# Kernel tuning notes

Hardware: AMD Instinct MI355X
Metric: run time of the kernel (lower is better)

The kernel has to match this reference:

```python
import jax, jax.numpy as jnp
import numpy as np

B, H, S, Dh = 4, 16, 2048, 64
NEG = -1.0e9


def setup_inputs() -> dict:
    key = jax.random.key(0)
    kq, kk, kv = jax.random.split(key, 3)
    q = jax.random.normal(kq, (B, H, S, Dh), dtype=jnp.float32)
    k = jax.random.normal(kk, (B, H, S, Dh), dtype=jnp.float32)
    v = jax.random.normal(kv, (B, H, S, Dh), dtype=jnp.float32)
    # causal mask: 1.0 where attention is disallowed (j > i), matching mask * -1e9
    mask = jnp.triu(jnp.ones((S, S), dtype=jnp.float32), k=1)[None, None, :, :]
    return {"q": q, "k": k, "v": v, "mask": mask}


def reference(q, k, v, mask):
    # scaled dot-product attention: softmax(QK^T / sqrt(Dh) + mask * -1e9) V
    dim_k = jnp.asarray(k.shape[-1], dtype=jnp.float32)
    logits = jnp.einsum("bhsd,bhtd->bhst", q, k) / jnp.sqrt(dim_k)
    logits = logits + mask * NEG
    weights = jax.nn.softmax(logits, axis=-1)
    return jnp.einsum("bhst,bhtd->bhsd", weights, v)
```

## Files before the change

kernel.cpp:

```cpp
#include <hip/hip_runtime.h>

#define S_LEN 2048
#define DH 64

typedef float f32x4 __attribute__((ext_vector_type(4)));
typedef __bf16 bf16x8 __attribute__((ext_vector_type(8)));

#define PTS 72

__device__ __forceinline__ unsigned short f2bf(float f) {
    unsigned u = __builtin_bit_cast(unsigned, f);
    u += 0x7fffu + ((u >> 16) & 1u);
    return (unsigned short)(u >> 16);
}

__device__ __forceinline__ uint4 pack8(const float* s) {
    unsigned short h[8];
#pragma unroll
    for (int i = 0; i < 8; ++i) h[i] = f2bf(s[i]);
    return *(const uint4*)h;
}

__device__ __forceinline__ unsigned pack_tr(float a, float b) {
    return __builtin_amdgcn_perm(__builtin_bit_cast(unsigned, b),
                                 __builtin_bit_cast(unsigned, a), 0x07060302u);
}

__device__ __forceinline__ bf16x8 ld128(const unsigned short* p) {
    return __builtin_bit_cast(bf16x8, *(const uint4*)p);
}

__global__ __launch_bounds__(256) void prep_kv(const float* __restrict__ k,
                                               const float* __restrict__ v,
                                               uint4* __restrict__ kimg,
                                               uint4* __restrict__ vimg) {
    __shared__ unsigned short tr[64 * 40];
    const int bid = blockIdx.x;
    const int t = threadIdx.x;
    if (bid < 4096) {
        const int r = t >> 3, b = t & 7;
        const int srcblk = b ^ (r & 7);
        const float* src = k + ((size_t)bid * 32 + r) * 64 + srcblk * 8;
        float buf[8];
        *(float4*)&buf[0] = *(const float4*)src;
        *(float4*)&buf[4] = *(const float4*)(src + 4);
        kimg[(size_t)bid * 256 + t] = pack8(buf);
    } else {
        const int vb = bid - 4096;
        const int r = t >> 3, cb = t & 7;
        const float* src = v + ((size_t)vb * 32 + r) * 64 + cb * 8;
        float buf[8];
        *(float4*)&buf[0] = *(const float4*)src;
        *(float4*)&buf[4] = *(const float4*)(src + 4);
#pragma unroll
        for (int i = 0; i < 8; ++i)
            tr[(cb * 8 + i) * 40 + r] = f2bf(buf[i]);
        __syncthreads();
        const int d = t >> 2, kb = t & 3;
        const int skb = kb ^ ((d >> 1) & 3);
        vimg[(size_t)vb * 256 + t] = *(const uint4*)&tr[d * 40 + skb * 8];
    }
}

template <int DIAG>
__device__ __forceinline__ void body64(
    const unsigned short* __restrict__ kt, const unsigned short* __restrict__ vt,
    unsigned short* __restrict__ pw0, unsigned short* __restrict__ pw1,
    const bf16x8* qf, f32x4 acc[2][4], f32x4* accl,
    int jt, int qbase, int quad, int c)
{
    const int sw = c & 7;
    const unsigned ones_u = 0x3F803F80u;
    uint4 ou; ou.x = ones_u; ou.y = ones_u; ou.z = ones_u; ou.w = ones_u;
    const bf16x8 ones = __builtin_bit_cast(bf16x8, ou);
    const int MTN = (DIAG == 1) ? 2 : 4;

#pragma unroll
    for (int mt = 0; mt < MTN; ++mt) {
        const unsigned short* kr = kt + (mt * 16 + c) * 64;
        bf16x8 ka0 = ld128(kr + ((quad ^ sw) << 3));
        bf16x8 ka1 = ld128(kr + (((quad | 4) ^ sw) << 3));
        f32x4 s0 = (f32x4){0.f, 0.f, 0.f, 0.f};
        f32x4 s1 = (f32x4){0.f, 0.f, 0.f, 0.f};
        s0 = __builtin_amdgcn_mfma_f32_16x16x32_bf16(ka0, qf[0], s0, 0, 0, 0);
        s0 = __builtin_amdgcn_mfma_f32_16x16x32_bf16(ka1, qf[1], s0, 0, 0, 0);
        s1 = __builtin_amdgcn_mfma_f32_16x16x32_bf16(ka0, qf[2], s1, 0, 0, 0);
        s1 = __builtin_amdgcn_mfma_f32_16x16x32_bf16(ka1, qf[3], s1, 0, 0, 0);

        const bool MASKMT = (DIAG == 1) || (DIAG == 2 && mt >= 2);
#pragma unroll
        for (int s = 0; s < 2; ++s) {
            const f32x4 st = s ? s1 : s0;
            const int ig = qbase + s * 16 + c;
            float p[4];
#pragma unroll
            for (int r = 0; r < 4; ++r) {
                float e = exp2f(st[r]);
                if (MASKMT) {
                    const int jg = jt * 64 + mt * 16 + quad * 4 + r;
                    e = (jg > ig) ? 0.f : e;
                }
                p[r] = e;
            }
            unsigned a = pack_tr(p[0], p[1]);
            unsigned b = pack_tr(p[2], p[3]);
            unsigned* pb = (unsigned*)(s ? pw1 : pw0) + c * (PTS / 2) + mt * 8 + quad * 2;
            *(uint2*)pb = make_uint2(a, b);
        }
    }

    bf16x8 pf00 = ld128(pw0 + c * PTS + quad * 8);
    bf16x8 pf10 = ld128(pw1 + c * PTS + quad * 8);
    accl[0] = __builtin_amdgcn_mfma_f32_16x16x32_bf16(pf00, ones, accl[0], 0, 0, 0);
    accl[1] = __builtin_amdgcn_mfma_f32_16x16x32_bf16(pf10, ones, accl[1], 0, 0, 0);
    bf16x8 pf01, pf11;
    if (DIAG != 1) {
        pf01 = ld128(pw0 + c * PTS + 32 + quad * 8);
        pf11 = ld128(pw1 + c * PTS + 32 + quad * 8);
        accl[0] = __builtin_amdgcn_mfma_f32_16x16x32_bf16(pf01, ones, accl[0], 0, 0, 0);
        accl[1] = __builtin_amdgcn_mfma_f32_16x16x32_bf16(pf11, ones, accl[1], 0, 0, 0);
    }

    const int vsw = (c >> 1) & 3;
#pragma unroll
    for (int dc = 0; dc < 4; ++dc) {
        const unsigned short* vr = vt + (dc * 16 + c) * 32 + ((quad ^ vsw) << 3);
        bf16x8 vf0 = ld128(vr);
        acc[0][dc] = __builtin_amdgcn_mfma_f32_16x16x32_bf16(pf00, vf0, acc[0][dc], 0, 0, 0);
        acc[1][dc] = __builtin_amdgcn_mfma_f32_16x16x32_bf16(pf10, vf0, acc[1][dc], 0, 0, 0);
        if (DIAG != 1) {
            bf16x8 vf1 = ld128(vr + 2048);
            acc[0][dc] = __builtin_amdgcn_mfma_f32_16x16x32_bf16(pf01, vf1, acc[0][dc], 0, 0, 0);
            acc[1][dc] = __builtin_amdgcn_mfma_f32_16x16x32_bf16(pf11, vf1, acc[1][dc], 0, 0, 0);
        }
    }
}

__global__ __launch_bounds__(256, 4) void fa_kernel(
    const float* __restrict__ q,
    const uint4* __restrict__ kimg,
    const uint4* __restrict__ vimg,
    float* __restrict__ out)
{
    __shared__ unsigned short kt[64 * 64];
    __shared__ unsigned short vt[2 * 64 * 32];
    __shared__ unsigned short pt[4][2][16 * PTS];

    const int tid  = threadIdx.x;
    const int lane = tid & 63;
    const int wave = tid >> 6;
    const int quad = lane >> 4;
    const int c    = lane & 15;

    const int bid  = blockIdx.x;
    const int bh   = bid & 63;
    const int qblk = bid >> 6;

    const int wt      = qblk * 4 + wave;
    const int qbase   = wt * 32;
    const int my_diag = wt >> 1;
    const int jt_last = 2 * qblk + 1;

    const size_t head_off = (size_t)bh * S_LEN * DH;

    const float SCALE = 0.125f * 1.4426950408889634f;
    bf16x8 qf[4];
#pragma unroll
    for (int s = 0; s < 2; ++s) {
        const float* qrow = q + head_off + (size_t)(qbase + s * 16 + c) * DH;
        float t0[8], t1[8];
#pragma unroll
        for (int i = 0; i < 8; ++i) t0[i] = qrow[quad * 8 + i] * SCALE;
#pragma unroll
        for (int i = 0; i < 8; ++i) t1[i] = qrow[32 + quad * 8 + i] * SCALE;
        qf[s * 2 + 0] = __builtin_bit_cast(bf16x8, pack8(t0));
        qf[s * 2 + 1] = __builtin_bit_cast(bf16x8, pack8(t1));
    }

    f32x4 acc[2][4];
#pragma unroll
    for (int s = 0; s < 2; ++s)
#pragma unroll
        for (int dc = 0; dc < 4; ++dc) acc[s][dc] = (f32x4){0.f, 0.f, 0.f, 0.f};
    f32x4 accl[2];
    accl[0] = (f32x4){0.f, 0.f, 0.f, 0.f};
    accl[1] = (f32x4){0.f, 0.f, 0.f, 0.f};

    const uint4* kin = kimg + (size_t)bh * 64 * 256 + tid;
    const uint4* vin = vimg + (size_t)bh * 64 * 256 + tid;
    unsigned short* pw0 = pt[wave][0];
    unsigned short* pw1 = pt[wave][1];

    uint4 kA = kin[0], kB = kin[256];
    uint4 vA = vin[0], vB = vin[256];
    for (int jt = 0; jt <= jt_last; ++jt) {
        __syncthreads();
        ((uint4*)kt)[tid] = kA;  ((uint4*)kt)[tid + 256] = kB;
        ((uint4*)vt)[tid] = vA;  ((uint4*)vt)[tid + 256] = vB;
        if (jt < jt_last) {
            kA = kin[(jt + 1) * 512];  kB = kin[(jt + 1) * 512 + 256];
            vA = vin[(jt + 1) * 512];  vB = vin[(jt + 1) * 512 + 256];
        }
        __syncthreads();

        if (jt < my_diag) {
            body64<0>(kt, vt, pw0, pw1, qf, acc, accl, jt, qbase, quad, c);
        } else if (jt == my_diag) {
            if ((wt & 1) == 0)
                body64<1>(kt, vt, pw0, pw1, qf, acc, accl, jt, qbase, quad, c);
            else
                body64<2>(kt, vt, pw0, pw1, qf, acc, accl, jt, qbase, quad, c);
        }
    }

    float* ob = out + head_off;
#pragma unroll
    for (int s = 0; s < 2; ++s) {
        float linv[4];
#pragma unroll
        for (int r = 0; r < 4; ++r) linv[r] = 1.0f / accl[s][r];
#pragma unroll
        for (int dc = 0; dc < 4; ++dc)
#pragma unroll
            for (int r = 0; r < 4; ++r) {
                const size_t idx =
                    (size_t)(qbase + s * 16 + quad * 4 + r) * DH + dc * 16 + c;
                ob[idx] = acc[s][dc][r] * linv[r];
            }
    }
}

#define KT_STRIDE 88
#define VT_STRIDE 36
__global__ __launch_bounds__(256) void fa_kernel_fb(
    const float* __restrict__ q, const float* __restrict__ k,
    const float* __restrict__ v, float* __restrict__ out)
{
    __shared__ unsigned short kts[32 * KT_STRIDE];
    __shared__ unsigned short vts[64 * VT_STRIDE];
    __shared__ unsigned short pts[4][16 * 40];
    const int tid = threadIdx.x, lane = tid & 63, wave = tid >> 6;
    const int quad = lane >> 4, c = lane & 15;
    const int bid = blockIdx.x, bh = bid & 63, qblk = 31 - (bid >> 6);
    const int qtile = qblk * 4 + wave, qbase = qtile * 16;
    const int my_diag = qtile >> 1, jt_last = (qblk * 4 + 3) >> 1;
    const size_t head_off = (size_t)bh * S_LEN * DH;
    const float* qrow = q + head_off + (size_t)(qbase + c) * DH;
    float qtmp[8];
#pragma unroll
    for (int i = 0; i < 8; ++i) qtmp[i] = qrow[quad * 8 + i];
    bf16x8 qf0 = __builtin_bit_cast(bf16x8, pack8(qtmp));
#pragma unroll
    for (int i = 0; i < 8; ++i) qtmp[i] = qrow[32 + quad * 8 + i];
    bf16x8 qf1 = __builtin_bit_cast(bf16x8, pack8(qtmp));
    f32x4 acc[4];
#pragma unroll
    for (int dc = 0; dc < 4; ++dc) acc[dc] = (f32x4){0.f, 0.f, 0.f, 0.f};
    float m_run = -1e30f, l_run = 0.f;
    const int ig = qbase + c;
    const int srow = tid >> 3, sdb = tid & 7;
    const int vcol = (((srow >> 3) ^ (sdb & 3)) << 3) | (srow & 7);
    const float LOG2E = 1.4426950408889634f;
    for (int jt = 0; jt <= jt_last; ++jt) {
        __syncthreads();
        {
            const size_t g = head_off + (size_t)(jt * 32 + srow) * DH + sdb * 8;
            float kbuf[8];
            *(float4*)&kbuf[0] = *(const float4*)(k + g);
            *(float4*)&kbuf[4] = *(const float4*)(k + g + 4);
            *(uint4*)&kts[srow * KT_STRIDE + sdb * 8] = pack8(kbuf);
            float vbuf[8];
            *(float4*)&vbuf[0] = *(const float4*)(v + g);
            *(float4*)&vbuf[4] = *(const float4*)(v + g + 4);
#pragma unroll
            for (int i = 0; i < 8; ++i)
                vts[(sdb * 8 + i) * VT_STRIDE + vcol] = f2bf(vbuf[i]);
        }
        __syncthreads();
        if (jt > my_diag) continue;
        f32x4 st[2];
#pragma unroll
        for (int mt = 0; mt < 2; ++mt) {
            const unsigned short* krow = &kts[(mt * 16 + c) * KT_STRIDE + quad * 8];
            bf16x8 ka0 = __builtin_bit_cast(bf16x8, *(const uint4*)krow);
            bf16x8 ka1 = __builtin_bit_cast(bf16x8, *(const uint4*)(krow + 32));
            f32x4 a = (f32x4){0.f, 0.f, 0.f, 0.f};
            a = __builtin_amdgcn_mfma_f32_16x16x32_bf16(ka0, qf0, a, 0, 0, 0);
            a = __builtin_amdgcn_mfma_f32_16x16x32_bf16(ka1, qf1, a, 0, 0, 0);
            st[mt] = a;
        }
        float tv[8];
#pragma unroll
        for (int mt = 0; mt < 2; ++mt)
#pragma unroll
            for (int r = 0; r < 4; ++r) {
                const int jg = jt * 32 + mt * 16 + quad * 4 + r;
                const float s = st[mt][r] * 0.125f;
                tv[mt * 4 + r] = (jg > ig) ? -1e30f : s;
            }
        float tm = tv[0];
#pragma unroll
        for (int i = 1; i < 8; ++i) tm = fmaxf(tm, tv[i]);
        tm = fmaxf(tm, __shfl_xor(tm, 16, 64));
        tm = fmaxf(tm, __shfl_xor(tm, 32, 64));
        const float m_new = fmaxf(m_run, tm);
        const float mb = m_new * LOG2E;
        float p[8], ps = 0.f;
#pragma unroll
        for (int i = 0; i < 8; ++i) { p[i] = exp2f(tv[i] * LOG2E - mb); ps += p[i]; }
        ps += __shfl_xor(ps, 16, 64);
        ps += __shfl_xor(ps, 32, 64);
        const float alpha = exp2f((m_run - m_new) * LOG2E);
        l_run = l_run * alpha + ps;
        m_run = m_new;
        unsigned short* pwf = pts[wave];
#pragma unroll
        for (int mt = 0; mt < 2; ++mt)
#pragma unroll
            for (int r = 0; r < 4; ++r)
                pwf[c * 40 + mt * 16 + quad * 4 + r] = f2bf(p[mt * 4 + r]);
        float ar[4];
#pragma unroll
        for (int r = 0; r < 4; ++r)
            ar[r] = __shfl(alpha, (quad << 4) + quad * 4 + r, 64);
#pragma unroll
        for (int dc = 0; dc < 4; ++dc)
#pragma unroll
            for (int r = 0; r < 4; ++r) acc[dc][r] *= ar[r];
        bf16x8 pf = __builtin_bit_cast(bf16x8, *(const uint4*)&pwf[c * 40 + quad * 8]);
#pragma unroll
        for (int dc = 0; dc < 4; ++dc) {
            const int vrow = dc * 16 + c;
            const int blk = quad ^ ((vrow >> 3) & 3);
            const unsigned short* vp = &vts[vrow * VT_STRIDE + blk * 8];
            uint2 a0 = *(const uint2*)vp;
            uint2 a1 = *(const uint2*)(vp + 4);
            uint4 u; u.x = a0.x; u.y = a0.y; u.z = a1.x; u.w = a1.y;
            bf16x8 vf = __builtin_bit_cast(bf16x8, u);
            acc[dc] = __builtin_amdgcn_mfma_f32_16x16x32_bf16(pf, vf, acc[dc], 0, 0, 0);
        }
    }
    float linv[4];
#pragma unroll
    for (int r = 0; r < 4; ++r) {
        const float lr = __shfl(l_run, (quad << 4) + quad * 4 + r, 64);
        linv[r] = 1.0f / lr;
    }
    float* ob = out + head_off;
#pragma unroll
    for (int dc = 0; dc < 4; ++dc)
#pragma unroll
        for (int r = 0; r < 4; ++r) {
            const size_t idx = (size_t)(qbase + quad * 4 + r) * DH + dc * 16 + c;
            ob[idx] = acc[dc][r] * linv[r];
        }
}

extern "C" void kernel_launch(void* const* d_in, const int* in_sizes, int n_in,
                              void* d_out, int out_size, void* d_ws, size_t ws_size,
                              hipStream_t stream) {
    const float* q = (const float*)d_in[0];
    const float* k = (const float*)d_in[1];
    const float* v = (const float*)d_in[2];
    float* o = (float*)d_out;
    const size_t need = (size_t)2 * 64 * 64 * 4096;
    if (ws_size >= need) {
        uint4* kimg = (uint4*)d_ws;
        uint4* vimg = kimg + (size_t)64 * 64 * 256;
        hipLaunchKernelGGL(prep_kv, dim3(8192), dim3(256), 0, stream, k, v, kimg, vimg);
        hipLaunchKernelGGL(fa_kernel, dim3(1024), dim3(256), 0, stream, q, kimg, vimg, o);
    } else {
        hipLaunchKernelGGL(fa_kernel_fb, dim3(2048), dim3(256), 0, stream, q, k, v, o);
    }
}
```

Baseline: 209.0 us.

## Pair low and high query tiles per wave to balance causal work

Each wave now owns two 16-row query tiles, one near the start of the sequence and its mirror near the end, instead of two adjacent tiles. Every wave and block therefore does about the same number of key blocks under the causal mask, which removes the imbalance where late query blocks did far more work than early ones. Diagonal handling is rewritten with per-16-row masking modes and single-tile bodies. The cost is more code paths and branching, and every block now loads K/V up to the hi tile's diagonal while the lo tile drops out early, running single-tile bodies with less MFMA reuse.

```diff
diff --git a/kernel.cpp b/kernel.cpp
--- a/kernel.cpp
+++ b/kernel.cpp
@@ -7,6 +7,7 @@
 typedef __bf16 bf16x8 __attribute__((ext_vector_type(8)));
 
 #define PTS 72
+#define MFMA16(A, B, C) __builtin_amdgcn_mfma_f32_16x16x32_bf16(A, B, C, 0, 0, 0)
 
 __device__ __forceinline__ unsigned short f2bf(float f) {
     unsigned u = __builtin_bit_cast(unsigned, f);
@@ -28,6 +29,11 @@
 
 __device__ __forceinline__ bf16x8 ld128(const unsigned short* p) {
     return __builtin_bit_cast(bf16x8, *(const uint4*)p);
+}
+
+__device__ __forceinline__ bf16x8 ones8() {
+    uint4 ou; ou.x = 0x3F803F80u; ou.y = ou.x; ou.z = ou.x; ou.w = ou.x;
+    return __builtin_bit_cast(bf16x8, ou);
 }
 
 __global__ __launch_bounds__(256) void prep_kv(const float* __restrict__ k,
@@ -62,77 +68,102 @@
     }
 }
 
-template <int DIAG>
-__device__ __forceinline__ void body64(
+__device__ __forceinline__ void body_pair(
     const unsigned short* __restrict__ kt, const unsigned short* __restrict__ vt,
     unsigned short* __restrict__ pw0, unsigned short* __restrict__ pw1,
-    const bf16x8* qf, f32x4 acc[2][4], f32x4* accl,
+    const bf16x8* qf, f32x4 acc[2][4], f32x4* accl, int quad, int c)
+{
+    const int sw = c & 7;
+    const bf16x8 ones = ones8();
+#pragma unroll
+    for (int mt = 0; mt < 4; ++mt) {
+        const unsigned short* kr = kt + (mt * 16 + c) * 64;
+        bf16x8 ka0 = ld128(kr + ((quad ^ sw) << 3));
+        bf16x8 ka1 = ld128(kr + (((quad | 4) ^ sw) << 3));
+        f32x4 s0 = (f32x4){0.f, 0.f, 0.f, 0.f};
+        f32x4 s1 = (f32x4){0.f, 0.f, 0.f, 0.f};
+        s0 = MFMA16(ka0, qf[0], s0);  s0 = MFMA16(ka1, qf[1], s0);
+        s1 = MFMA16(ka0, qf[2], s1);  s1 = MFMA16(ka1, qf[3], s1);
+#pragma unroll
+        for (int s = 0; s < 2; ++s) {
+            const f32x4 st = s ? s1 : s0;
+            float p0 = exp2f(st[0]), p1 = exp2f(st[1]);
+            float p2 = exp2f(st[2]), p3 = exp2f(st[3]);
+            unsigned* pb = (unsigned*)(s ? pw1 : pw0) + c * (PTS / 2) + mt * 8 + quad * 2;
+            *(uint2*)pb = make_uint2(pack_tr(p0, p1), pack_tr(p2, p3));
+        }
+    }
+    bf16x8 pf00 = ld128(pw0 + c * PTS + quad * 8);
+    bf16x8 pf10 = ld128(pw1 + c * PTS + quad * 8);
+    bf16x8 pf01 = ld128(pw0 + c * PTS + 32 + quad * 8);
+    bf16x8 pf11 = ld128(pw1 + c * PTS + 32 + quad * 8);
+    accl[0] = MFMA16(pf00, ones, accl[0]);  accl[0] = MFMA16(pf01, ones, accl[0]);
+    accl[1] = MFMA16(pf10, ones, accl[1]);  accl[1] = MFMA16(pf11, ones, accl[1]);
+    const int vsw = (c >> 1) & 3;
+#pragma unroll
+    for (int dc = 0; dc < 4; ++dc) {
+        const unsigned short* vr = vt + (dc * 16 + c) * 32 + ((quad ^ vsw) << 3);
+        bf16x8 vf0 = ld128(vr);
+        bf16x8 vf1 = ld128(vr + 2048);
+        acc[0][dc] = MFMA16(pf00, vf0, acc[0][dc]);
+        acc[0][dc] = MFMA16(pf01, vf1, acc[0][dc]);
+        acc[1][dc] = MFMA16(pf10, vf0, acc[1][dc]);
+        acc[1][dc] = MFMA16(pf11, vf1, acc[1][dc]);
+    }
+}
+
+template <int MODE>
+__device__ __forceinline__ void body_one(
+    const unsigned short* __restrict__ kt, const unsigned short* __restrict__ vt,
+    unsigned short* __restrict__ pw,
+    bf16x8 qfA, bf16x8 qfB, f32x4* acc4, f32x4& accl,
     int jt, int qbase, int quad, int c)
 {
     const int sw = c & 7;
-    const unsigned ones_u = 0x3F803F80u;
-    uint4 ou; ou.x = ones_u; ou.y = ones_u; ou.z = ones_u; ou.w = ones_u;
-    const bf16x8 ones = __builtin_bit_cast(bf16x8, ou);
-    const int MTN = (DIAG == 1) ? 2 : 4;
-
+    const bf16x8 ones = ones8();
+    constexpr int MTN = (MODE < 0) ? 4 : (MODE + 1);
 #pragma unroll
     for (int mt = 0; mt < MTN; ++mt) {
         const unsigned short* kr = kt + (mt * 16 + c) * 64;
         bf16x8 ka0 = ld128(kr + ((quad ^ sw) << 3));
         bf16x8 ka1 = ld128(kr + (((quad | 4) ^ sw) << 3));
         f32x4 s0 = (f32x4){0.f, 0.f, 0.f, 0.f};
-        f32x4 s1 = (f32x4){0.f, 0.f, 0.f, 0.f};
-        s0 = __builtin_amdgcn_mfma_f32_16x16x32_bf16(ka0, qf[0], s0, 0, 0, 0);
-        s0 = __builtin_amdgcn_mfma_f32_16x16x32_bf16(ka1, qf[1], s0, 0, 0, 0);
-        s1 = __builtin_amdgcn_mfma_f32_16x16x32_bf16(ka0, qf[2], s1, 0, 0, 0);
-        s1 = __builtin_amdgcn_mfma_f32_16x16x32_bf16(ka1, qf[3], s1, 0, 0, 0);
-
-        const bool MASKMT = (DIAG == 1) || (DIAG == 2 && mt >= 2);
-#pragma unroll
-        for (int s = 0; s < 2; ++s) {
-            const f32x4 st = s ? s1 : s0;
-            const int ig = qbase + s * 16 + c;
-            float p[4];
-#pragma unroll
-            for (int r = 0; r < 4; ++r) {
-                float e = exp2f(st[r]);
-                if (MASKMT) {
-                    const int jg = jt * 64 + mt * 16 + quad * 4 + r;
-                    e = (jg > ig) ? 0.f : e;
-                }
-                p[r] = e;
+        s0 = MFMA16(ka0, qfA, s0);  s0 = MFMA16(ka1, qfB, s0);
+        float p[4];
+        const int ig = qbase + c;
+#pragma unroll
+        for (int r = 0; r < 4; ++r) {
+            float e = exp2f(s0[r]);
+            if (MODE >= 0 && mt == MODE) {
+                const int jg = jt * 64 + mt * 16 + quad * 4 + r;
+                e = (jg > ig) ? 0.f : e;
             }
-            unsigned a = pack_tr(p[0], p[1]);
-            unsigned b = pack_tr(p[2], p[3]);
-            unsigned* pb = (unsigned*)(s ? pw1 : pw0) + c * (PTS / 2) + mt * 8 + quad * 2;
-            *(uint2*)pb = make_uint2(a, b);
-        }
-    }
-
-    bf16x8 pf00 = ld128(pw0 + c * PTS + quad * 8);
-    bf16x8 pf10 = ld128(pw1 + c * PTS + quad * 8);
-    accl[0] = __builtin_amdgcn_mfma_f32_16x16x32_bf16(pf00, ones, accl[0], 0, 0, 0);
-    accl[1] = __builtin_amdgcn_mfma_f32_16x16x32_bf16(pf10, ones, accl[1], 0, 0, 0);
-    bf16x8 pf01, pf11;
-    if (DIAG != 1) {
-        pf01 = ld128(pw0 + c * PTS + 32 + quad * 8);
-        pf11 = ld128(pw1 + c * PTS + 32 + quad * 8);
-        accl[0] = __builtin_amdgcn_mfma_f32_16x16x32_bf16(pf01, ones, accl[0], 0, 0, 0);
-        accl[1] = __builtin_amdgcn_mfma_f32_16x16x32_bf16(pf11, ones, accl[1], 0, 0, 0);
-    }
-
+            p[r] = e;
+        }
+        unsigned* pb = (unsigned*)pw + c * (PTS / 2) + mt * 8 + quad * 2;
+        *(uint2*)pb = make_uint2(pack_tr(p[0], p[1]), pack_tr(p[2], p[3]));
+    }
+    if (MODE >= 0) {
+#pragma unroll
+        for (int mt = MODE + 1; mt < 4; ++mt) {
+            unsigned* pb = (unsigned*)pw + c * (PTS / 2) + mt * 8 + quad * 2;
+            *(uint2*)pb = make_uint2(0u, 0u);
+        }
+    }
+    constexpr bool CH1 = (MODE < 0) || (MODE >= 2);
+    bf16x8 pf0 = ld128(pw + c * PTS + quad * 8);
+    accl = MFMA16(pf0, ones, accl);
+    bf16x8 pf1 = pf0;
+    if (CH1) {
+        pf1 = ld128(pw + c * PTS + 32 + quad * 8);
+        accl = MFMA16(pf1, ones, accl);
+    }
     const int vsw = (c >> 1) & 3;
 #pragma unroll
     for (int dc = 0; dc < 4; ++dc) {
         const unsigned short* vr = vt + (dc * 16 + c) * 32 + ((quad ^ vsw) << 3);
-        bf16x8 vf0 = ld128(vr);
-        acc[0][dc] = __builtin_amdgcn_mfma_f32_16x16x32_bf16(pf00, vf0, acc[0][dc], 0, 0, 0);
-        acc[1][dc] = __builtin_amdgcn_mfma_f32_16x16x32_bf16(pf10, vf0, acc[1][dc], 0, 0, 0);
-        if (DIAG != 1) {
-            bf16x8 vf1 = ld128(vr + 2048);
-            acc[0][dc] = __builtin_amdgcn_mfma_f32_16x16x32_bf16(pf01, vf1, acc[0][dc], 0, 0, 0);
-            acc[1][dc] = __builtin_amdgcn_mfma_f32_16x16x32_bf16(pf11, vf1, acc[1][dc], 0, 0, 0);
-        }
+        acc4[dc] = MFMA16(pf0, ld128(vr), acc4[dc]);
+        if (CH1) acc4[dc] = MFMA16(pf1, ld128(vr + 2048), acc4[dc]);
     }
 }
 
@@ -152,14 +183,19 @@
     const int quad = lane >> 4;
     const int c    = lane & 15;
 
-    const int bid  = blockIdx.x;
-    const int bh   = bid & 63;
-    const int qblk = bid >> 6;
-
-    const int wt      = qblk * 4 + wave;
-    const int qbase   = wt * 32;
-    const int my_diag = wt >> 1;
-    const int jt_last = 2 * qblk + 1;
+    const int bid = blockIdx.x;
+    const int bh  = bid & 63;
+    const int pg  = bid >> 6;
+
+    const int p       = pg * 4 + wave;
+    const int hi      = 127 - p;
+    const int lo_diag = p >> 2;
+    const int hi_diag = hi >> 2;
+    const int blk_last = (127 - pg * 4) >> 2;
+    const int qbase_lo = p * 16;
+    const int qbase_hi = hi * 16;
+    const int S3lo = p & 3;
+    const int S3hi = 3 - S3lo;
 
     const size_t head_off = (size_t)bh * S_LEN * DH;
 
@@ -167,7 +203,8 @@
     bf16x8 qf[4];
 #pragma unroll
     for (int s = 0; s < 2; ++s) {
-        const float* qrow = q + head_off + (size_t)(qbase + s * 16 + c) * DH;
+        const int qb = s ? qbase_hi : qbase_lo;
+        const float* qrow = q + head_off + (size_t)(qb + c) * DH;
         float t0[8], t1[8];
 #pragma unroll
         for (int i = 0; i < 8; ++i) t0[i] = qrow[quad * 8 + i] * SCALE;
@@ -193,29 +230,42 @@
 
     uint4 kA = kin[0], kB = kin[256];
     uint4 vA = vin[0], vB = vin[256];
-    for (int jt = 0; jt <= jt_last; ++jt) {
+    for (int jt = 0; jt <= blk_last; ++jt) {
         __syncthreads();
         ((uint4*)kt)[tid] = kA;  ((uint4*)kt)[tid + 256] = kB;
         ((uint4*)vt)[tid] = vA;  ((uint4*)vt)[tid + 256] = vB;
-        if (jt < jt_last) {
+        if (jt < blk_last) {
             kA = kin[(jt + 1) * 512];  kB = kin[(jt + 1) * 512 + 256];
             vA = vin[(jt + 1) * 512];  vB = vin[(jt + 1) * 512 + 256];
         }
         __syncthreads();
 
-        if (jt < my_diag) {
-            body64<0>(kt, vt, pw0, pw1, qf, acc, accl, jt, qbase, quad, c);
-        } else if (jt == my_diag) {
-            if ((wt & 1) == 0)
-                body64<1>(kt, vt, pw0, pw1, qf, acc, accl, jt, qbase, quad, c);
-            else
-                body64<2>(kt, vt, pw0, pw1, qf, acc, accl, jt, qbase, quad, c);
+        if (jt < lo_diag) {
+            body_pair(kt, vt, pw0, pw1, qf, acc, accl, quad, c);
+        } else if (jt == lo_diag) {
+            body_one<-1>(kt, vt, pw1, qf[2], qf[3], acc[1], accl[1], jt, qbase_hi, quad, c);
+            switch (S3lo) {
+                case 0: body_one<0>(kt, vt, pw0, qf[0], qf[1], acc[0], accl[0], jt, qbase_lo, quad, c); break;
+                case 1: body_one<1>(kt, vt, pw0, qf[0], qf[1], acc[0], accl[0], jt, qbase_lo, quad, c); break;
+                case 2: body_one<2>(kt, vt, pw0, qf[0], qf[1], acc[0], accl[0], jt, qbase_lo, quad, c); break;
+                default: body_one<3>(kt, vt, pw0, qf[0], qf[1], acc[0], accl[0], jt, qbase_lo, quad, c); break;
+            }
+        } else if (jt < hi_diag) {
+            body_one<-1>(kt, vt, pw1, qf[2], qf[3], acc[1], accl[1], jt, qbase_hi, quad, c);
+        } else if (jt == hi_diag) {
+            switch (S3hi) {
+                case 0: body_one<0>(kt, vt, pw1, qf[2], qf[3], acc[1], accl[1], jt, qbase_hi, quad, c); break;
+                case 1: body_one<1>(kt, vt, pw1, qf[2], qf[3], acc[1], accl[1], jt, qbase_hi, quad, c); break;
+                case 2: body_one<2>(kt, vt, pw1, qf[2], qf[3], acc[1], accl[1], jt, qbase_hi, quad, c); break;
+                default: body_one<3>(kt, vt, pw1, qf[2], qf[3], acc[1], accl[1], jt, qbase_hi, quad, c); break;
+            }
         }
     }
 
     float* ob = out + head_off;
 #pragma unroll
     for (int s = 0; s < 2; ++s) {
+        const int qb = s ? qbase_hi : qbase_lo;
         float linv[4];
 #pragma unroll
         for (int r = 0; r < 4; ++r) linv[r] = 1.0f / accl[s][r];
@@ -223,8 +273,7 @@
         for (int dc = 0; dc < 4; ++dc)
 #pragma unroll
             for (int r = 0; r < 4; ++r) {
-                const size_t idx =
-                    (size_t)(qbase + s * 16 + quad * 4 + r) * DH + dc * 16 + c;
+                const size_t idx = (size_t)(qb + quad * 4 + r) * DH + dc * 16 + c;
                 ob[idx] = acc[s][dc][r] * linv[r];
             }
     }
@@ -285,8 +334,8 @@
             bf16x8 ka0 = __builtin_bit_cast(bf16x8, *(const uint4*)krow);
             bf16x8 ka1 = __builtin_bit_cast(bf16x8, *(const uint4*)(krow + 32));
             f32x4 a = (f32x4){0.f, 0.f, 0.f, 0.f};
-            a = __builtin_amdgcn_mfma_f32_16x16x32_bf16(ka0, qf0, a, 0, 0, 0);
-            a = __builtin_amdgcn_mfma_f32_16x16x32_bf16(ka1, qf1, a, 0, 0, 0);
+            a = MFMA16(ka0, qf0, a);
+            a = MFMA16(ka1, qf1, a);
             st[mt] = a;
         }
         float tv[8];
@@ -337,7 +386,7 @@
             uint2 a1 = *(const uint2*)(vp + 4);
             uint4 u; u.x = a0.x; u.y = a0.y; u.z = a1.x; u.w = a1.y;
             bf16x8 vf = __builtin_bit_cast(bf16x8, u);
-            acc[dc] = __builtin_amdgcn_mfma_f32_16x16x32_bf16(pf, vf, acc[dc], 0, 0, 0);
+            acc[dc] = MFMA16(pf, vf, acc[dc]);
         }
     }
     float linv[4];
```

Result: slower. 311.8 us (+49.2%).
